# Optimization experiments

Measured on AMD Instinct MI355X. Metric: run time of the kernel, lower is better.

The kernel has to match this reference:

```python
import jax, jax.numpy as jnp
import numpy as np

B, S, D, H = 2, 4096, 512, 8
DK = D // H  # 64

def setup_inputs() -> dict:
    key = jax.random.key(0)
    k1, k2, k3, k4 = jax.random.split(key, 4)
    return {
        "queries": jax.random.normal(k1, (B, S, D), dtype=jnp.float32),
        "keys": jax.random.normal(k2, (B, S, D), dtype=jnp.float32),
        "values": jax.random.normal(k3, (B, S, D), dtype=jnp.float32),
        "W_o": jax.random.normal(k4, (D, D), dtype=jnp.float32) * (1.0 / np.sqrt(D)),
        "b_o": jnp.zeros((D,), dtype=jnp.float32),
    }

def reference(queries, keys, values, W_o, b_o):
    b_s, nq, _ = queries.shape
    nk = keys.shape[1]
    # split heads: (b, s, h, dk) -> (b, h, s, dk)
    q = queries.reshape(b_s, nq, H, DK).transpose(0, 2, 1, 3)
    k = keys.reshape(b_s, nk, H, DK).transpose(0, 2, 1, 3)
    v = values.reshape(b_s, nk, H, DK).transpose(0, 2, 1, 3)
    # full (nq, nk) attention matrix, scaled by sqrt(d_k)
    att = jnp.einsum("bhqd,bhkd->bhqk", q, k) / np.sqrt(DK).astype(np.float32)
    att = jax.nn.softmax(att, axis=-1)  # dropout is identity at inference
    out = jnp.einsum("bhqk,bhkd->bhqd", att, v)
    out = out.transpose(0, 2, 1, 3).reshape(b_s, nq, H * DK)
    return out @ W_o + b_o
```

## Files before the change

### kernel.cpp

```cpp
#include <hip/hip_runtime.h>
#include <hip/hip_bf16.h>

#define Bn 2
#define Sn 4096
#define Dn 512
#define Hn 8

typedef _Float16 f16x8 __attribute__((ext_vector_type(8)));
typedef __fp16 fp16x2 __attribute__((ext_vector_type(2)));
typedef float f32x16 __attribute__((ext_vector_type(16)));
typedef unsigned uint2v __attribute__((ext_vector_type(2)));

#if __has_builtin(__builtin_amdgcn_global_load_lds)
#define HAS_GLL 1
typedef const __attribute__((address_space(1))) unsigned int* gas1_t;
typedef __attribute__((address_space(3))) unsigned int* las3_t;
static __device__ __forceinline__ void ld_lds16(const void* g, void* l) {
    __builtin_amdgcn_global_load_lds((gas1_t)g, (las3_t)l, 16, 0, 0);
}
#else
#define HAS_GLL 0
#endif

static __device__ __forceinline__ unsigned pkh(float a, float b) {
    union { fp16x2 h; unsigned u; } r;
    r.h = __builtin_amdgcn_cvt_pkrtz(a, b);
    return r.u;
}

static __device__ __forceinline__ f16x8 xchg2(unsigned g0x, unsigned g0y,
                                              unsigned g1x, unsigned g1y, int hi) {
    union { unsigned u[4]; f16x8 v; } f;
#if __has_builtin(__builtin_amdgcn_permlane32_swap)
    uint2v rx = __builtin_amdgcn_permlane32_swap(g0x, g1x, false, false);
    uint2v ry = __builtin_amdgcn_permlane32_swap(g0y, g1y, false, false);
    f.u[0] = rx.x; f.u[1] = ry.x; f.u[2] = rx.y; f.u[3] = ry.y;
#else
    int sx = hi ? (int)g0x : (int)g1x;
    int sy = hi ? (int)g0y : (int)g1y;
    int rx = __shfl_xor(sx, 32);
    int ry = __shfl_xor(sy, 32);
    unsigned ox = hi ? g1x : g0x;
    unsigned oy = hi ? g1y : g0y;
    f.u[0] = hi ? (unsigned)rx : ox;
    f.u[1] = hi ? (unsigned)ry : oy;
    f.u[2] = hi ? ox : (unsigned)rx;
    f.u[3] = hi ? oy : (unsigned)ry;
#endif
    return f.v;
}

__global__ __launch_bounds__(256) void prep_kernel(
    const float* __restrict__ K, const float* __restrict__ V, const float* __restrict__ W,
    unsigned short* __restrict__ Kb, unsigned short* __restrict__ Vb,
    unsigned short* __restrict__ Wb) {
    const int vb = blockIdx.x;
    const int tid = threadIdx.x;
    if (vb < 1024) {
        const int kt = vb & 63, bh = vb >> 6;
        const int b = bh >> 3, h = bh & 7;
        unsigned short* dst = Kb + ((size_t)bh * 64 + kt) * 4096;
#pragma unroll
        for (int i = 0; i < 2; ++i) {
            int c = tid + i * 256;
            int f = c >> 6, ln = c & 63;
            int ktile = f >> 2, ks = f & 3;
            int row = ktile * 32 + (ln & 31);
            int dk = ks * 16 + (ln >> 5) * 8;
            const float* src = K + ((size_t)(b * Sn + kt * 64 + row)) * Dn + h * 64 + dk;
            float4 a0 = *(const float4*)src;
            float4 a1 = *(const float4*)(src + 4);
            uint4 o;
            o.x = pkh(a0.x, a0.y); o.y = pkh(a0.z, a0.w);
            o.z = pkh(a1.x, a1.y); o.w = pkh(a1.z, a1.w);
            *(uint4*)(dst + c * 8) = o;
        }
    } else if (vb < 2048) {
        const int u = vb - 1024;
        const int kt = u & 63, bh = u >> 6;
        const int b = bh >> 3, h = bh & 7;
        unsigned short* dst = Vb + ((size_t)bh * 64 + kt) * 4096;
#pragma unroll
        for (int i = 0; i < 2; ++i) {
            int c = tid + i * 256;
            int f = c >> 6, ln = c & 63;
            int dt = f >> 2, ks = f & 3;
            int dk = dt * 32 + (ln & 31);
            int key0 = ks * 16 + (ln >> 5) * 8;
            const float* src = V + ((size_t)(b * Sn + kt * 64 + key0)) * Dn + h * 64 + dk;
            uint4 o;
            o.x = pkh(src[0 * Dn], src[1 * Dn]);
            o.y = pkh(src[2 * Dn], src[3 * Dn]);
            o.z = pkh(src[4 * Dn], src[5 * Dn]);
            o.w = pkh(src[6 * Dn], src[7 * Dn]);
            *(uint4*)(dst + c * 8) = o;
        }
    } else {
        int c = (vb - 2048) * 256 + tid;
        int ln = c & 63, f = c >> 6;
        int ntile = f >> 5, ks = f & 31;
        int n = ntile * 32 + (ln & 31);
        int k0 = ks * 16 + (ln >> 5) * 8;
        uint4 o;
        o.x = pkh(W[(size_t)(k0 + 0) * Dn + n], W[(size_t)(k0 + 1) * Dn + n]);
        o.y = pkh(W[(size_t)(k0 + 2) * Dn + n], W[(size_t)(k0 + 3) * Dn + n]);
        o.z = pkh(W[(size_t)(k0 + 4) * Dn + n], W[(size_t)(k0 + 5) * Dn + n]);
        o.w = pkh(W[(size_t)(k0 + 6) * Dn + n], W[(size_t)(k0 + 7) * Dn + n]);
        *(uint4*)(Wb + c * 8) = o;
    }
}

__global__ __launch_bounds__(256, 2) void attn_kernel(
    const float* __restrict__ Q,
    const unsigned short* __restrict__ Kb,
    const unsigned short* __restrict__ Vb,
    unsigned short* __restrict__ ObA) {
    __shared__ __align__(16) unsigned short KV[16384];

    const int qt = blockIdx.x;
    const int bh = blockIdx.y;
    const int b = bh >> 3, h = bh & 7;
    const int tid = threadIdx.x;
    const int w = tid >> 6;
    const int lane = tid & 63;
    const int q = lane & 31;
    const int hi = lane >> 5;
    const int q0 = qt * 128 + w * 32;
    const float cexp = 0.18033688f;

    f16x8 qf[4];
    {
        const float* qp = Q + ((size_t)(b * Sn + q0 + q)) * Dn + h * 64 + hi * 8;
#pragma unroll
        for (int ks = 0; ks < 4; ++ks) {
            float4 a0 = *(const float4*)(qp + ks * 16);
            float4 a1 = *(const float4*)(qp + ks * 16 + 4);
            union { unsigned u[4]; f16x8 v; } f;
            f.u[0] = pkh(a0.x * cexp, a0.y * cexp);
            f.u[1] = pkh(a0.z * cexp, a0.w * cexp);
            f.u[2] = pkh(a1.x * cexp, a1.y * cexp);
            f.u[3] = pkh(a1.z * cexp, a1.w * cexp);
            qf[ks] = f.v;
        }
    }

    f32x16 zf;
#pragma unroll
    for (int r = 0; r < 16; ++r) zf[r] = 0.f;
    f32x16 oacc[2];
    oacc[0] = zf; oacc[1] = zf;
    float l_ = 0.f;

    f16x8 va[8];
    f16x8 pb[4];

    const size_t tbase = (size_t)bh * 64 * 4096;
    const unsigned short* kgw = Kb + tbase + w * 1024;
    const unsigned short* vgw = Vb + tbase + w * 1024;
    const int lK = w * 1024;
    const int lV = 4096 + w * 1024;

#if HAS_GLL
#define STAGE(itx, bb) { \
    const unsigned short* ksp = kgw + (size_t)(itx) * 4096 + lane * 8; \
    const unsigned short* vsp = vgw + (size_t)(itx) * 4096 + lane * 8; \
    unsigned short* lk = &KV[(bb) * 8192 + lK]; \
    unsigned short* lv = &KV[(bb) * 8192 + lV]; \
    ld_lds16(ksp, lk); ld_lds16(ksp + 512, lk + 512); \
    ld_lds16(vsp, lv); ld_lds16(vsp + 512, lv + 512); }
#else
#define STAGE(itx, bb) { \
    const unsigned short* ksp = Kb + tbase + (size_t)(itx) * 4096; \
    const unsigned short* vsp = Vb + tbase + (size_t)(itx) * 4096; \
    uint4 a0 = *(const uint4*)(ksp + tid * 8); \
    uint4 a1 = *(const uint4*)(ksp + 2048 + tid * 8); \
    uint4 a2 = *(const uint4*)(vsp + tid * 8); \
    uint4 a3 = *(const uint4*)(vsp + 2048 + tid * 8); \
    unsigned short* lk = &KV[(bb) * 8192]; \
    unsigned short* lv = lk + 4096; \
    *(uint4*)&lk[tid * 8] = a0; *(uint4*)&lk[2048 + tid * 8] = a1; \
    *(uint4*)&lv[tid * 8] = a2; *(uint4*)&lv[2048 + tid * 8] = a3; }
#endif

    auto TILE = [&](const unsigned short* Kbuf) {
        const unsigned short* Vbuf = Kbuf + 4096;
        f32x16 sa0, sa1;
        {
            f16x8 ka = *(const f16x8*)&Kbuf[0 * 512 + lane * 8];
            f16x8 kb = *(const f16x8*)&Kbuf[4 * 512 + lane * 8];
            sa0 = __builtin_amdgcn_mfma_f32_32x32x16_f16(ka, qf[0], zf, 0, 0, 0);
            sa1 = __builtin_amdgcn_mfma_f32_32x32x16_f16(kb, qf[0], zf, 0, 0, 0);
#pragma unroll
            for (int ks = 1; ks < 4; ++ks) {
                ka = *(const f16x8*)&Kbuf[(0 + ks) * 512 + lane * 8];
                kb = *(const f16x8*)&Kbuf[(4 + ks) * 512 + lane * 8];
                sa0 = __builtin_amdgcn_mfma_f32_32x32x16_f16(ka, qf[ks], sa0, 0, 0, 0);
                sa1 = __builtin_amdgcn_mfma_f32_32x32x16_f16(kb, qf[ks], sa1, 0, 0, 0);
            }
        }
        float e0[16], e1[16];
        float s0 = 0.f, s1 = 0.f;
#pragma unroll
        for (int r = 0; r < 16; ++r) { e0[r] = __builtin_amdgcn_exp2f(sa0[r]); s0 += e0[r]; }
#pragma unroll
        for (int r = 0; r < 16; ++r) { e1[r] = __builtin_amdgcn_exp2f(sa1[r]); s1 += e1[r]; }
        l_ += s0 + s1;
#pragma unroll
        for (int kp = 0; kp < 4; ++kp) {
            const float* e = (kp < 2) ? e0 : e1;
            const int s2 = kp & 1;
            unsigned g0x = pkh(e[8 * s2 + 0], e[8 * s2 + 1]);
            unsigned g0y = pkh(e[8 * s2 + 2], e[8 * s2 + 3]);
            unsigned g1x = pkh(e[8 * s2 + 4], e[8 * s2 + 5]);
            unsigned g1y = pkh(e[8 * s2 + 6], e[8 * s2 + 7]);
            pb[kp] = xchg2(g0x, g0y, g1x, g1y, hi);
        }
#pragma unroll
        for (int kp = 0; kp < 4; ++kp) {
            va[kp]     = *(const f16x8*)&Vbuf[(0 + kp) * 512 + lane * 8];
            va[4 + kp] = *(const f16x8*)&Vbuf[(4 + kp) * 512 + lane * 8];
        }
    };

#define PV() { \
    _Pragma("unroll") \
    for (int kp = 0; kp < 4; ++kp) { \
        oacc[0] = __builtin_amdgcn_mfma_f32_32x32x16_f16(va[kp], pb[kp], oacc[0], 0, 0, 0); \
        oacc[1] = __builtin_amdgcn_mfma_f32_32x32x16_f16(va[4 + kp], pb[kp], oacc[1], 0, 0, 0); } }

    STAGE(0, 0);
    __syncthreads();
    STAGE(1, 1);
    TILE(&KV[0]);

    for (int it = 1; it < 64; ++it) {
        __syncthreads();
        if (it < 63) STAGE(it + 1, (it + 1) & 1);
        const unsigned short* Kbuf = &KV[(it & 1) * 8192];
        PV();
        TILE(Kbuf);
    }
    PV();

    l_ += __shfl_xor(l_, 32);
    const float li = 1.f / l_;
    const int gm = b * 128 + qt * 4 + w;
#pragma unroll
    for (int ksg = 0; ksg < 4; ++ksg) {
        const int dt = ksg >> 1, k2 = ksg & 1;
        unsigned g0x = pkh(oacc[dt][8 * k2 + 0] * li, oacc[dt][8 * k2 + 1] * li);
        unsigned g0y = pkh(oacc[dt][8 * k2 + 2] * li, oacc[dt][8 * k2 + 3] * li);
        unsigned g1x = pkh(oacc[dt][8 * k2 + 4] * li, oacc[dt][8 * k2 + 5] * li);
        unsigned g1y = pkh(oacc[dt][8 * k2 + 6] * li, oacc[dt][8 * k2 + 7] * li);
        f16x8 frag = xchg2(g0x, g0y, g1x, g1y, hi);
        union { f16x8 v; uint4 u; } fu; fu.v = frag;
        *(uint4*)&ObA[((size_t)(gm * 32 + h * 4 + ksg) * 64 + lane) * 8] = fu.u;
    }
}

__global__ __launch_bounds__(256) void proj_kernel(
    const unsigned short* __restrict__ ObA,
    const unsigned short* __restrict__ Wb,
    const float* __restrict__ bias,
    float* __restrict__ out) {
    __shared__ __align__(16) unsigned short Ash[8192];
    __shared__ __align__(16) unsigned short Wsh[4096];

    const int mt = blockIdx.x;
    const int nt = blockIdx.y;
    const int tid = threadIdx.x;
    const int w = tid >> 6;
    const int lane = tid & 63;
    const int q = lane & 31;
    const int hi = lane >> 5;

    f32x16 acc[2];
#pragma unroll
    for (int t = 0; t < 2; ++t)
#pragma unroll
        for (int r = 0; r < 16; ++r) acc[t][r] = 0.f;

    for (int kt = 0; kt < 8; ++kt) {
        __syncthreads();
#pragma unroll
        for (int i = 0; i < 4; ++i) {
            int ci = (tid >> 6) + i * 4;
            int ml = ci >> 2, ksl = ci & 3;
            *(uint4*)&Ash[ci * 512 + lane * 8] =
                *(const uint4*)(ObA + (((size_t)(mt * 4 + ml) * 32 + kt * 4 + ksl) * 64 + lane) * 8);
        }
#pragma unroll
        for (int i = 0; i < 2; ++i) {
            int ci = (tid >> 6) + i * 4;
            int ntl = ci >> 2, ksl = ci & 3;
            *(uint4*)&Wsh[ci * 512 + lane * 8] =
                *(const uint4*)(Wb + (((size_t)(nt * 2 + ntl) * 32 + kt * 4 + ksl) * 64 + lane) * 8);
        }
        __syncthreads();

#pragma unroll
        for (int ks = 0; ks < 4; ++ks) {
            f16x8 a  = *(const f16x8*)&Ash[(w * 4 + ks) * 512 + lane * 8];
            f16x8 b0 = *(const f16x8*)&Wsh[(0 * 4 + ks) * 512 + lane * 8];
            f16x8 b1 = *(const f16x8*)&Wsh[(4 + ks) * 512 + lane * 8];
            acc[0] = __builtin_amdgcn_mfma_f32_32x32x16_f16(a, b0, acc[0], 0, 0, 0);
            acc[1] = __builtin_amdgcn_mfma_f32_32x32x16_f16(a, b1, acc[1], 0, 0, 0);
        }
    }

#pragma unroll
    for (int ntl = 0; ntl < 2; ++ntl) {
        int col = nt * 64 + ntl * 32 + q;
        float bv = bias[col];
#pragma unroll
        for (int reg = 0; reg < 16; ++reg) {
            int row = mt * 128 + w * 32 + (reg & 3) + 8 * (reg >> 2) + 4 * hi;
            out[(size_t)row * Dn + col] = acc[ntl][reg] + bv;
        }
    }
}

extern "C" void kernel_launch(void* const* d_in, const int* in_sizes, int n_in,
                              void* d_out, int out_size, void* d_ws, size_t ws_size,
                              hipStream_t stream) {
    const float* Q = (const float*)d_in[0];
    const float* K = (const float*)d_in[1];
    const float* V = (const float*)d_in[2];
    const float* W = (const float*)d_in[3];
    const float* bo = (const float*)d_in[4];
    float* out = (float*)d_out;

    char* ws = (char*)d_ws;
    unsigned short* Kb  = (unsigned short*)(ws);
    unsigned short* Vb  = (unsigned short*)(ws + 8388608);
    unsigned short* Wb  = (unsigned short*)(ws + 16777216);
    unsigned short* ObA = (unsigned short*)(ws + 17301504);

    prep_kernel<<<2176, 256, 0, stream>>>(K, V, W, Kb, Vb, Wb);
    attn_kernel<<<dim3(32, 16), 256, 0, stream>>>(Q, Kb, Vb, ObA);
    proj_kernel<<<dim3(64, 8), 256, 0, stream>>>(ObA, Wb, bo, out);
}
```

Baseline: 184.3 us.

## Software-pipeline QK MFMA of next tile with exp2 of previous scores

```diff
diff --git a/kernel.cpp b/kernel.cpp
--- a/kernel.cpp
+++ b/kernel.cpp
@@ -151,8 +151,8 @@
     oacc[0] = zf; oacc[1] = zf;
     float l_ = 0.f;
 
+    f32x16 saP0, saP1;
     f16x8 va[8];
-    f16x8 pb[4];
 
     const size_t tbase = (size_t)bh * 64 * 4096;
     const unsigned short* kgw = Kb + tbase + w * 1024;
@@ -182,32 +182,72 @@
     *(uint4*)&lv[tid * 8] = a2; *(uint4*)&lv[2048 + tid * 8] = a3; }
 #endif
 
-    auto TILE = [&](const unsigned short* Kbuf) {
+    STAGE(0, 0);
+    __syncthreads();
+    STAGE(1, 1);
+    {
+        const unsigned short* Kbuf = &KV[0];
         const unsigned short* Vbuf = Kbuf + 4096;
-        f32x16 sa0, sa1;
+        f16x8 ka = *(const f16x8*)&Kbuf[0 * 512 + lane * 8];
+        f16x8 kb = *(const f16x8*)&Kbuf[4 * 512 + lane * 8];
+        saP0 = __builtin_amdgcn_mfma_f32_32x32x16_f16(ka, qf[0], zf, 0, 0, 0);
+        saP1 = __builtin_amdgcn_mfma_f32_32x32x16_f16(kb, qf[0], zf, 0, 0, 0);
+#pragma unroll
+        for (int ks = 1; ks < 4; ++ks) {
+            ka = *(const f16x8*)&Kbuf[(0 + ks) * 512 + lane * 8];
+            kb = *(const f16x8*)&Kbuf[(4 + ks) * 512 + lane * 8];
+            saP0 = __builtin_amdgcn_mfma_f32_32x32x16_f16(ka, qf[ks], saP0, 0, 0, 0);
+            saP1 = __builtin_amdgcn_mfma_f32_32x32x16_f16(kb, qf[ks], saP1, 0, 0, 0);
+        }
+#pragma unroll
+        for (int kp = 0; kp < 4; ++kp) {
+            va[kp]     = *(const f16x8*)&Vbuf[(0 + kp) * 512 + lane * 8];
+            va[4 + kp] = *(const f16x8*)&Vbuf[(4 + kp) * 512 + lane * 8];
+        }
+    }
+
+#pragma unroll 2
+    for (int it = 1; it < 64; ++it) {
+        __syncthreads();
+        if (it < 63) STAGE(it + 1, (it + 1) & 1);
+        const unsigned short* Kbuf = &KV[(it & 1) * 8192];
+        const unsigned short* Vbuf = Kbuf + 4096;
+
+        float ep[32];
+        float t0 = 0.f, t1 = 0.f, t2 = 0.f, t3 = 0.f;
+        f32x16 sb0, sb1;
         {
             f16x8 ka = *(const f16x8*)&Kbuf[0 * 512 + lane * 8];
             f16x8 kb = *(const f16x8*)&Kbuf[4 * 512 + lane * 8];
-            sa0 = __builtin_amdgcn_mfma_f32_32x32x16_f16(ka, qf[0], zf, 0, 0, 0);
-            sa1 = __builtin_amdgcn_mfma_f32_32x32x16_f16(kb, qf[0], zf, 0, 0, 0);
-#pragma unroll
-            for (int ks = 1; ks < 4; ++ks) {
-                ka = *(const f16x8*)&Kbuf[(0 + ks) * 512 + lane * 8];
-                kb = *(const f16x8*)&Kbuf[(4 + ks) * 512 + lane * 8];
-                sa0 = __builtin_amdgcn_mfma_f32_32x32x16_f16(ka, qf[ks], sa0, 0, 0, 0);
-                sa1 = __builtin_amdgcn_mfma_f32_32x32x16_f16(kb, qf[ks], sa1, 0, 0, 0);
-            }
-        }
-        float e0[16], e1[16];
-        float s0 = 0.f, s1 = 0.f;
-#pragma unroll
-        for (int r = 0; r < 16; ++r) { e0[r] = __builtin_amdgcn_exp2f(sa0[r]); s0 += e0[r]; }
-#pragma unroll
-        for (int r = 0; r < 16; ++r) { e1[r] = __builtin_amdgcn_exp2f(sa1[r]); s1 += e1[r]; }
-        l_ += s0 + s1;
-#pragma unroll
-        for (int kp = 0; kp < 4; ++kp) {
-            const float* e = (kp < 2) ? e0 : e1;
+            sb0 = __builtin_amdgcn_mfma_f32_32x32x16_f16(ka, qf[0], zf, 0, 0, 0);
+            sb1 = __builtin_amdgcn_mfma_f32_32x32x16_f16(kb, qf[0], zf, 0, 0, 0);
+#pragma unroll
+            for (int r = 0; r < 8; ++r) { ep[r] = __builtin_amdgcn_exp2f(saP0[r]); t0 += ep[r]; }
+            ka = *(const f16x8*)&Kbuf[1 * 512 + lane * 8];
+            kb = *(const f16x8*)&Kbuf[5 * 512 + lane * 8];
+            sb0 = __builtin_amdgcn_mfma_f32_32x32x16_f16(ka, qf[1], sb0, 0, 0, 0);
+            sb1 = __builtin_amdgcn_mfma_f32_32x32x16_f16(kb, qf[1], sb1, 0, 0, 0);
+#pragma unroll
+            for (int r = 0; r < 8; ++r) { ep[8 + r] = __builtin_amdgcn_exp2f(saP0[8 + r]); t1 += ep[8 + r]; }
+            ka = *(const f16x8*)&Kbuf[2 * 512 + lane * 8];
+            kb = *(const f16x8*)&Kbuf[6 * 512 + lane * 8];
+            sb0 = __builtin_amdgcn_mfma_f32_32x32x16_f16(ka, qf[2], sb0, 0, 0, 0);
+            sb1 = __builtin_amdgcn_mfma_f32_32x32x16_f16(kb, qf[2], sb1, 0, 0, 0);
+#pragma unroll
+            for (int r = 0; r < 8; ++r) { ep[16 + r] = __builtin_amdgcn_exp2f(saP1[r]); t2 += ep[16 + r]; }
+            ka = *(const f16x8*)&Kbuf[3 * 512 + lane * 8];
+            kb = *(const f16x8*)&Kbuf[7 * 512 + lane * 8];
+            sb0 = __builtin_amdgcn_mfma_f32_32x32x16_f16(ka, qf[3], sb0, 0, 0, 0);
+            sb1 = __builtin_amdgcn_mfma_f32_32x32x16_f16(kb, qf[3], sb1, 0, 0, 0);
+#pragma unroll
+            for (int r = 0; r < 8; ++r) { ep[24 + r] = __builtin_amdgcn_exp2f(saP1[8 + r]); t3 += ep[24 + r]; }
+        }
+        l_ += (t0 + t1) + (t2 + t3);
+
+        f16x8 pb[4];
+#pragma unroll
+        for (int kp = 0; kp < 4; ++kp) {
+            const float* e = (kp < 2) ? ep : (ep + 16);
             const int s2 = kp & 1;
             unsigned g0x = pkh(e[8 * s2 + 0], e[8 * s2 + 1]);
             unsigned g0y = pkh(e[8 * s2 + 2], e[8 * s2 + 3]);
@@ -217,30 +257,42 @@
         }
 #pragma unroll
         for (int kp = 0; kp < 4; ++kp) {
+            oacc[0] = __builtin_amdgcn_mfma_f32_32x32x16_f16(va[kp], pb[kp], oacc[0], 0, 0, 0);
+            oacc[1] = __builtin_amdgcn_mfma_f32_32x32x16_f16(va[4 + kp], pb[kp], oacc[1], 0, 0, 0);
+        }
+#pragma unroll
+        for (int kp = 0; kp < 4; ++kp) {
             va[kp]     = *(const f16x8*)&Vbuf[(0 + kp) * 512 + lane * 8];
             va[4 + kp] = *(const f16x8*)&Vbuf[(4 + kp) * 512 + lane * 8];
         }
-    };
-
-#define PV() { \
-    _Pragma("unroll") \
-    for (int kp = 0; kp < 4; ++kp) { \
-        oacc[0] = __builtin_amdgcn_mfma_f32_32x32x16_f16(va[kp], pb[kp], oacc[0], 0, 0, 0); \
-        oacc[1] = __builtin_amdgcn_mfma_f32_32x32x16_f16(va[4 + kp], pb[kp], oacc[1], 0, 0, 0); } }
-
-    STAGE(0, 0);
-    __syncthreads();
-    STAGE(1, 1);
-    TILE(&KV[0]);
-
-    for (int it = 1; it < 64; ++it) {
-        __syncthreads();
-        if (it < 63) STAGE(it + 1, (it + 1) & 1);
-        const unsigned short* Kbuf = &KV[(it & 1) * 8192];
-        PV();
-        TILE(Kbuf);
-    }
-    PV();
+        saP0 = sb0; saP1 = sb1;
+    }
+
+    {
+        float ep[32];
+        float t0 = 0.f, t1 = 0.f, t2 = 0.f, t3 = 0.f;
+#pragma unroll
+        for (int r = 0; r < 8; ++r) { ep[r] = __builtin_amdgcn_exp2f(saP0[r]); t0 += ep[r]; }
+#pragma unroll
+        for (int r = 0; r < 8; ++r) { ep[8 + r] = __builtin_amdgcn_exp2f(saP0[8 + r]); t1 += ep[8 + r]; }
+#pragma unroll
+        for (int r = 0; r < 8; ++r) { ep[16 + r] = __builtin_amdgcn_exp2f(saP1[r]); t2 += ep[16 + r]; }
+#pragma unroll
+        for (int r = 0; r < 8; ++r) { ep[24 + r] = __builtin_amdgcn_exp2f(saP1[8 + r]); t3 += ep[24 + r]; }
+        l_ += (t0 + t1) + (t2 + t3);
+#pragma unroll
+        for (int kp = 0; kp < 4; ++kp) {
+            const float* e = (kp < 2) ? ep : (ep + 16);
+            const int s2 = kp & 1;
+            unsigned g0x = pkh(e[8 * s2 + 0], e[8 * s2 + 1]);
+            unsigned g0y = pkh(e[8 * s2 + 2], e[8 * s2 + 3]);
+            unsigned g1x = pkh(e[8 * s2 + 4], e[8 * s2 + 5]);
+            unsigned g1y = pkh(e[8 * s2 + 6], e[8 * s2 + 7]);
+            f16x8 pb = xchg2(g0x, g0y, g1x, g1y, hi);
+            oacc[0] = __builtin_amdgcn_mfma_f32_32x32x16_f16(va[kp], pb, oacc[0], 0, 0, 0);
+            oacc[1] = __builtin_amdgcn_mfma_f32_32x32x16_f16(va[4 + kp], pb, oacc[1], 0, 0, 0);
+        }
+    }
 
     l_ += __shfl_xor(l_, 32);
     const float li = 1.f / l_;
```

New measurement: 186.2 us. About the same (+1.0%).
